# Kernel optimization log

Measured on AMD Instinct MI355X. Metric: run time of the kernel, lower is better.

The kernel has to match this reference:

```python
import jax, jax.numpy as jnp
import numpy as np

GB_TAU = 1.0
_NOISE_KEY = jax.random.key(42)


def setup_inputs() -> dict:
    key = jax.random.key(0)
    kq, kk, kv = jax.random.split(key, 3)
    n_genes, n_latent, d_k, n_cells = 16384, 4096, 64, 1024
    query = jax.random.normal(kq, (n_genes, d_k), dtype=jnp.float32)
    key_t = jax.random.normal(kk, (n_latent, d_k), dtype=jnp.float32)
    value = jax.random.normal(kv, (n_latent, n_cells), dtype=jnp.float32)
    return {"query": query, "key": key_t, "value": value}


def _gumbel_noise(shape, dtype):
    # standard Gumbel(0,1): -log(-log(U)), U ~ Uniform(0,1)
    u = jax.random.uniform(_NOISE_KEY, shape, dtype=dtype,
                           minval=jnp.finfo(dtype).tiny, maxval=1.0)
    return -jnp.log(-jnp.log(u))


def reference(query, key, value):
    d_k = query.shape[-1]
    # [n_genes, n_latent] scaled dot-product scores
    scores = jnp.matmul(query, key.T) / jnp.sqrt(jnp.asarray(d_k, query.dtype))
    # gumbel_softmax(hard=False): softmax((logits + g) / tau, axis=-1)
    g = _gumbel_noise(scores.shape, scores.dtype)
    p_attn = jax.nn.softmax((scores + g) / GB_TAU, axis=-1)
    out = jnp.matmul(p_attn, value)  # [n_genes, n_cells]
    return out, p_attn
```

## Files before the change

kernel.cpp:

```cpp
#include <hip/hip_runtime.h>
#include <cstdint>
#include <cstddef>

#define N_GENES  16384
#define N_LATENT 4096
#define D_K      64
#define N_CELLS  1024

#define NOISE_PARTITIONABLE 1

typedef __attribute__((ext_vector_type(8))) short bf16x8;
typedef __attribute__((ext_vector_type(4))) float f32x4;

__device__ __forceinline__ uint32_t rotl32(uint32_t x, int r) {
  return (x << r) | (x >> (32 - r));
}

__device__ __forceinline__ void threefry2x32(uint32_t c0, uint32_t c1,
                                             uint32_t& o0, uint32_t& o1) {
  const uint32_t ks0 = 0u, ks1 = 42u, ks2 = 0u ^ 42u ^ 0x1BD11BDAu;
  uint32_t x0 = c0 + ks0;
  uint32_t x1 = c1 + ks1;
#define TFR(r) { x0 += x1; x1 = rotl32(x1, r); x1 ^= x0; }
  TFR(13) TFR(15) TFR(26) TFR(6)
  x0 += ks1; x1 += ks2 + 1u;
  TFR(17) TFR(29) TFR(16) TFR(24)
  x0 += ks2; x1 += ks0 + 2u;
  TFR(13) TFR(15) TFR(26) TFR(6)
  x0 += ks0; x1 += ks1 + 3u;
  TFR(17) TFR(29) TFR(16) TFR(24)
  x0 += ks1; x1 += ks2 + 4u;
  TFR(13) TFR(15) TFR(26) TFR(6)
  x0 += ks2; x1 += ks0 + 5u;
#undef TFR
  o0 = x0; o1 = x1;
}

__device__ __forceinline__ uint32_t rand_bits(uint32_t m) {
#if NOISE_PARTITIONABLE
  uint32_t b0, b1;
  threefry2x32(0u, m, b0, b1);
  return b0 ^ b1;
#else
  const uint32_t h = 1u << 25;
  uint32_t b0, b1;
  if (m < h) { threefry2x32(m, m + h, b0, b1); return b0; }
  else       { threefry2x32(m - h, m, b0, b1); return b1; }
#endif
}

__device__ __forceinline__ float fastlog(float x) {
  float r;
  asm("v_log_f32 %0, %1" : "=v"(r) : "v"(x));
  return r * 0.69314718055994531f;
}

__device__ __forceinline__ float gumbel_noise(uint32_t m) {
  uint32_t bits = rand_bits(m);
  float f = __uint_as_float((bits >> 9) | 0x3f800000u) - 1.0f;
  float u = f + 1.17549435e-38f;
  float t = -fastlog(u);
  return -fastlog(t);
}

__device__ __forceinline__ ushort f2bf(float x) {
  uint32_t u = __float_as_uint(x);
  uint32_t r = (u + 0x7FFFu + ((u >> 16) & 1u)) >> 16;
  return (ushort)r;
}

__device__ __forceinline__ float bf2f(uint32_t us) {
  return __uint_as_float(us << 16);
}

__device__ __forceinline__ void split1(float x, ushort& h, ushort& l) {
  ushort hb = f2bf(x);
  float hf = __uint_as_float((uint32_t)hb << 16);
  h = hb;
  l = f2bf(x - hf);
}

__device__ __forceinline__ int swz(int row, int kcol) {
  return row * 64 + (((kcol >> 3) ^ (row & 7)) << 3) + (kcol & 7);
}

__global__ __launch_bounds__(256) void k_logexp(const float* __restrict__ Q,
                                                const float* __restrict__ Kk,
                                                ushort* __restrict__ Pe,
                                                float* __restrict__ Sp) {
  __shared__ ushort Qh[64 * 64], Ql[64 * 64], Kh[64 * 64], Kl[64 * 64];
  const int t = threadIdx.x;
  const int bm = blockIdx.x, bn = blockIdx.y;
  const float4* Q4 = (const float4*)(Q + ((size_t)bm << 12));
  const float4* K4 = (const float4*)(Kk + ((size_t)bn << 12));
#pragma unroll
  for (int i = 0; i < 4; ++i) {
    int idx = t + (i << 8);
    int r = idx >> 4;
    int k0 = (idx & 15) << 2;
    int sidx = swz(r, k0);
    float4 a = Q4[idx];
    ushort4 h, lo;
    split1(a.x * 0.125f, h.x, lo.x); split1(a.y * 0.125f, h.y, lo.y);
    split1(a.z * 0.125f, h.z, lo.z); split1(a.w * 0.125f, h.w, lo.w);
    *(ushort4*)&Qh[sidx] = h; *(ushort4*)&Ql[sidx] = lo;
    float4 b = K4[idx];
    split1(b.x, h.x, lo.x); split1(b.y, h.y, lo.y);
    split1(b.z, h.z, lo.z); split1(b.w, h.w, lo.w);
    *(ushort4*)&Kh[sidx] = h; *(ushort4*)&Kl[sidx] = lo;
  }
  __syncthreads();

  const int l = t & 63, w = t >> 6;
  const int wm = (w >> 1) << 5, wn = (w & 1) << 5;
  const int fr = l & 15;
  const int seg = l >> 4;
  const int koff = seg << 3;
  f32x4 acc[2][2] = {};
#pragma unroll
  for (int kseg = 0; kseg < 2; ++kseg) {
    bf16x8 ah[2], al[2], bh[2], bl[2];
    const int kc = kseg * 32 + koff;
#pragma unroll
    for (int m = 0; m < 2; ++m) {
      int row = wm + m * 16 + fr;
      int sidx = swz(row, kc);
      ah[m] = *(const bf16x8*)&Qh[sidx];
      al[m] = *(const bf16x8*)&Ql[sidx];
    }
#pragma unroll
    for (int n = 0; n < 2; ++n) {
      int row = wn + n * 16 + fr;
      int sidx = swz(row, kc);
      bh[n] = *(const bf16x8*)&Kh[sidx];
      bl[n] = *(const bf16x8*)&Kl[sidx];
    }
#pragma unroll
    for (int m = 0; m < 2; ++m)
#pragma unroll
      for (int n = 0; n < 2; ++n) {
        acc[m][n] = __builtin_amdgcn_mfma_f32_16x16x32_bf16(
            ah[m], bh[n], acc[m][n], 0, 0, 0);
        acc[m][n] = __builtin_amdgcn_mfma_f32_16x16x32_bf16(
            ah[m], bl[n], acc[m][n], 0, 0, 0);
        acc[m][n] = __builtin_amdgcn_mfma_f32_16x16x32_bf16(
            al[m], bh[n], acc[m][n], 0, 0, 0);
      }
  }

  const int gr0 = (bm << 6) + wm + (seg << 2);
  const int gc0 = (bn << 6) + wn + fr;
  float sloc[2][4] = {};
#pragma unroll
  for (int m = 0; m < 2; ++m)
#pragma unroll
    for (int n = 0; n < 2; ++n) {
      int col = gc0 + n * 16;
#pragma unroll
      for (int j = 0; j < 4; ++j) {
        int row = gr0 + m * 16 + j;
        uint32_t mb = (uint32_t)row * 4096u + (uint32_t)col;
        float e;
        asm("v_exp_f32 %0, %1" : "=v"(e)
            : "v"((acc[m][n][j] + gumbel_noise(mb)) * 1.4426950408889634f));
        Pe[(size_t)row * 4096 + col] = f2bf(e);
        sloc[m][j] += e;
      }
    }
  __shared__ float part[64][2];
#pragma unroll
  for (int m = 0; m < 2; ++m)
#pragma unroll
    for (int j = 0; j < 4; ++j) {
      float s = sloc[m][j];
      s += __shfl_xor(s, 1, 64); s += __shfl_xor(s, 2, 64);
      s += __shfl_xor(s, 4, 64); s += __shfl_xor(s, 8, 64);
      if (fr == 0) part[wm + m * 16 + (seg << 2) + j][wn >> 5] = s;
    }
  __syncthreads();
  if (t < 64)
    Sp[((size_t)(bm << 6) + t) * 64 + bn] = part[t][0] + part[t][1];
}

__global__ __launch_bounds__(256) void k_rowinv(const float* __restrict__ Sp,
                                                float* __restrict__ inv) {
  int r = blockIdx.x * 256 + threadIdx.x;
  const float4* s4 = (const float4*)(Sp + (size_t)r * 64);
  float s = 0.f;
#pragma unroll
  for (int i = 0; i < 16; ++i) {
    float4 v = s4[i];
    s += (v.x + v.y) + (v.z + v.w);
  }
  inv[r] = 1.0f / s;
}

__global__ __launch_bounds__(256) void k_pwrite(const ushort* __restrict__ Pe,
                                                const float* __restrict__ inv,
                                                float* __restrict__ P) {
  size_t i8 = (size_t)blockIdx.x * 256 + threadIdx.x;
  int row = (int)(i8 >> 9);
  float iv = inv[row];
  uint4 u = *(const uint4*)(Pe + i8 * 8);
  float4 o0, o1;
  o0.x = bf2f(u.x & 0xFFFFu) * iv; o0.y = bf2f(u.x >> 16) * iv;
  o0.z = bf2f(u.y & 0xFFFFu) * iv; o0.w = bf2f(u.y >> 16) * iv;
  o1.x = bf2f(u.z & 0xFFFFu) * iv; o1.y = bf2f(u.z >> 16) * iv;
  o1.z = bf2f(u.w & 0xFFFFu) * iv; o1.w = bf2f(u.w >> 16) * iv;
  *(float4*)(P + i8 * 8) = o0;
  *(float4*)(P + i8 * 8 + 4) = o1;
}

__global__ __launch_bounds__(256) void k_vt(const float* __restrict__ V,
                                            ushort* __restrict__ VT) {
  __shared__ ushort tile[64][68];
  const int t = threadIdx.x;
  const int k0 = blockIdx.x << 6, n0 = blockIdx.y << 6;
#pragma unroll
  for (int i = 0; i < 16; ++i) {
    int idx = t + (i << 8);
    int kr = idx >> 6;
    int c = idx & 63;
    tile[c][kr] = f2bf(V[(size_t)(k0 + kr) * 1024 + n0 + c]);
  }
  __syncthreads();
#pragma unroll
  for (int i = 0; i < 8; ++i) {
    int idx = t + (i << 8);
    int n = idx >> 5, kp = idx & 31;
    ushort2 o;
    o.x = tile[n][2 * kp];
    o.y = tile[n][2 * kp + 1];
    ((ushort2*)&VT[(size_t)(n0 + n) * 4096 + k0])[kp] = o;
  }
}

__device__ __forceinline__ void llds16(void* lds, const void* g) {
  __builtin_amdgcn_global_load_lds(
      (const __attribute__((address_space(1))) uint32_t*)g,
      (__attribute__((address_space(3))) uint32_t*)lds, 16, 0, 0);
}

__device__ __forceinline__ void stage_kt(ushort* ldsA, ushort* ldsB,
                                         const ushort* gA, const ushort* gB,
                                         int t) {
#pragma unroll
  for (int i = 0; i < 4; ++i) {
    int cid = (i << 9) + t;
    int row = cid >> 3, g = cid & 7;
    int gs = g ^ (row & 7);
    llds16(ldsA + (size_t)cid * 8, gA + (size_t)row * 4096 + gs * 8);
  }
#pragma unroll
  for (int i = 0; i < 4; ++i) {
    int cid = (i << 9) + t;
    int row = cid >> 3, g = cid & 7;
    int gs = g ^ (row & 7);
    llds16(ldsB + (size_t)cid * 8, gB + (size_t)row * 4096 + gs * 8);
  }
}

__global__ __launch_bounds__(512, 2) void k_pv3(const ushort* __restrict__ Pe,
                                                const ushort* __restrict__ VT,
                                                const float* __restrict__ inv,
                                                float* __restrict__ O) {
  __shared__ ushort lds[2][2][256 * 64];
  const int t = threadIdx.x;
  const int b = blockIdx.x;
  const int xcd = b & 7, idx = b >> 3;
  const int by = xcd * 8 + (idx >> 2);
  const int bx = idx & 3;
  const int base_m = by << 8, base_n = bx << 8;
  const int l = t & 63, w = t >> 6;
  const int wm = w >> 2, wn = w & 3;
  const int fr = l & 15, seg = l >> 4;

  const ushort* gA = Pe + (size_t)base_m * 4096;
  const ushort* gB = VT + (size_t)base_n * 4096;

  f32x4 acc[8][4] = {};

  stage_kt(lds[0][0], lds[0][1], gA, gB, t);

#define LDA_H(mh)                                                            \
  {                                                                          \
    _Pragma("unroll") for (int m = 0; m < 4; ++m)                            \
        _Pragma("unroll") for (int kk = 0; kk < 2; ++kk) {                   \
      int row = wm * 128 + (mh)*64 + m * 16 + fr;                            \
      a[m][kk] = *(const bf16x8*)&A[row * 64 +                               \
                                    ((((kk << 2) + seg) ^ (row & 7)) << 3)]; \
    }                                                                        \
  }
#define LDB_H(dst, nh)                                                       \
  {                                                                          \
    _Pragma("unroll") for (int n = 0; n < 2; ++n)                            \
        _Pragma("unroll") for (int kk = 0; kk < 2; ++kk) {                   \
      int row = wn * 64 + (nh)*32 + n * 16 + fr;                             \
      dst[n][kk] = *(const bf16x8*)&B[row * 64 +                             \
                                    ((((kk << 2) + seg) ^ (row & 7)) << 3)]; \
    }                                                                        \
  }
#define QUAD(mh, nh, bb)                                                     \
  {                                                                          \
    __builtin_amdgcn_s_setprio(1);                                           \
    _Pragma("unroll") for (int m = 0; m < 4; ++m)                            \
        _Pragma("unroll") for (int n = 0; n < 2; ++n)                        \
            _Pragma("unroll") for (int kk = 0; kk < 2; ++kk)                 \
        acc[(mh)*4 + m][(nh)*2 + n] = __builtin_amdgcn_mfma_f32_16x16x32_bf16( \
            a[m][kk], bb[n][kk], acc[(mh)*4 + m][(nh)*2 + n], 0, 0, 0);      \
    __builtin_amdgcn_s_setprio(0);                                           \
    __builtin_amdgcn_s_barrier();                                            \
  }

  for (int it = 0; it < 64; ++it) {
    const int slot = it & 1;
    const int ktn = (it < 63) ? it + 1 : it;
    stage_kt(lds[slot ^ 1][0], lds[slot ^ 1][1],
             gA + ktn * 64, gB + ktn * 64, t);
    asm volatile("s_waitcnt vmcnt(8)" ::: "memory");
    __builtin_amdgcn_s_barrier();
    const ushort* A = lds[slot][0];
    const ushort* B = lds[slot][1];
    bf16x8 a[4][2], b0[2][2], b1[2][2];
    LDA_H(0) LDB_H(b0, 0)
    QUAD(0, 0, b0)
    LDB_H(b1, 1)
    QUAD(0, 1, b1)
    LDA_H(1)
    QUAD(1, 0, b0)
    QUAD(1, 1, b1)
  }

#pragma unroll
  for (int mi = 0; mi < 8; ++mi) {
    int row_ = base_m + wm * 128 + mi * 16 + seg * 4;
#pragma unroll
    for (int j = 0; j < 4; ++j) {
      float iv = inv[row_ + j];
#pragma unroll
      for (int ni = 0; ni < 4; ++ni)
        O[(size_t)(row_ + j) * 1024 + base_n + wn * 64 + ni * 16 + fr] =
            acc[mi][ni][j] * iv;
    }
  }
#undef LDA_H
#undef LDB_H
#undef QUAD
}

__global__ __launch_bounds__(256) void k_logits_raw(const float* __restrict__ Q,
                                                    const float* __restrict__ Kk,
                                                    float* __restrict__ L) {
  __shared__ float Qt[64][68];
  __shared__ float Kt[64][68];
  const int t = threadIdx.x;
  const int bm = blockIdx.x, bn = blockIdx.y;
  const float4* Q4 = (const float4*)(Q + ((size_t)bm << 12));
  const float4* K4 = (const float4*)(Kk + ((size_t)bn << 12));
#pragma unroll
  for (int i = 0; i < 4; ++i) {
    int idx = t + (i << 8);
    int r = idx >> 4;
    int k0 = (idx & 15) << 2;
    float4 a = Q4[idx];
    Qt[k0 + 0][r] = a.x; Qt[k0 + 1][r] = a.y;
    Qt[k0 + 2][r] = a.z; Qt[k0 + 3][r] = a.w;
    float4 b = K4[idx];
    Kt[k0 + 0][r] = b.x; Kt[k0 + 1][r] = b.y;
    Kt[k0 + 2][r] = b.z; Kt[k0 + 3][r] = b.w;
  }
  __syncthreads();
  const int r0 = (t >> 4) << 2;
  const int c0 = (t & 15) << 2;
  float acc[4][4] = {};
#pragma unroll 8
  for (int k = 0; k < 64; ++k) {
    float a[4], b[4];
    *(float4*)a = *(const float4*)&Qt[k][r0];
    *(float4*)b = *(const float4*)&Kt[k][c0];
#pragma unroll
    for (int i = 0; i < 4; ++i)
#pragma unroll
      for (int j = 0; j < 4; ++j)
        acc[i][j] = fmaf(a[i], b[j], acc[i][j]);
  }
  const int gr = (bm << 6) + r0;
  const int gc = (bn << 6) + c0;
#pragma unroll
  for (int i = 0; i < 4; ++i) {
    uint32_t mb = (uint32_t)(gr + i) * 4096u + (uint32_t)gc;
    float4 o;
    o.x = acc[i][0] * 0.125f + gumbel_noise(mb + 0u);
    o.y = acc[i][1] * 0.125f + gumbel_noise(mb + 1u);
    o.z = acc[i][2] * 0.125f + gumbel_noise(mb + 2u);
    o.w = acc[i][3] * 0.125f + gumbel_noise(mb + 3u);
    *(float4*)&L[(size_t)(gr + i) * 4096 + gc] = o;
  }
}

__global__ __launch_bounds__(256) void k_softmax(float* __restrict__ P) {
  const int row = blockIdx.x;
  float* Lr = P + ((size_t)row << 12);
  const int t = threadIdx.x;
  float4 v[4];
#pragma unroll
  for (int i = 0; i < 4; ++i) v[i] = ((const float4*)Lr)[t + (i << 8)];
  float mx = -3.402823466e38f;
#pragma unroll
  for (int i = 0; i < 4; ++i)
    mx = fmaxf(mx, fmaxf(fmaxf(v[i].x, v[i].y), fmaxf(v[i].z, v[i].w)));
#pragma unroll
  for (int o = 1; o < 64; o <<= 1) mx = fmaxf(mx, __shfl_xor(mx, o, 64));
  __shared__ float redm[4];
  __shared__ float reds[4];
  const int lane = t & 63, w = t >> 6;
  if (lane == 0) redm[w] = mx;
  __syncthreads();
  mx = fmaxf(fmaxf(redm[0], redm[1]), fmaxf(redm[2], redm[3]));
  float s = 0.f;
#pragma unroll
  for (int i = 0; i < 4; ++i) {
    v[i].x = expf(v[i].x - mx); v[i].y = expf(v[i].y - mx);
    v[i].z = expf(v[i].z - mx); v[i].w = expf(v[i].w - mx);
    s += (v[i].x + v[i].y) + (v[i].z + v[i].w);
  }
#pragma unroll
  for (int o = 1; o < 64; o <<= 1) s += __shfl_xor(s, o, 64);
  if (lane == 0) reds[w] = s;
  __syncthreads();
  const float inv = 1.0f / (((reds[0] + reds[1]) + (reds[2] + reds[3])));
#pragma unroll
  for (int i = 0; i < 4; ++i) {
    v[i].x *= inv; v[i].y *= inv; v[i].z *= inv; v[i].w *= inv;
    ((float4*)Lr)[t + (i << 8)] = v[i];
  }
}

__global__ __launch_bounds__(256) void k_pv(const float* __restrict__ P,
                                            const float* __restrict__ V,
                                            float* __restrict__ O) {
  __shared__ float Pt[32][132];
  __shared__ float Vs[32][132];
  const int t = threadIdx.x;
  const int base_m = blockIdx.x << 7;
  const int base_n = blockIdx.y << 7;
  const int tr = (t >> 4) << 2;
  const int tc = (t & 15) << 2;
  float acc[2][2][4][4] = {};
  for (int k0 = 0; k0 < N_LATENT; k0 += 32) {
#pragma unroll
    for (int i = 0; i < 4; ++i) {
      int idx = t + (i << 8);
      int m = idx >> 3;
      int kk = (idx & 7) << 2;
      float4 a = *(const float4*)&P[(size_t)(base_m + m) * 4096 + (k0 + kk)];
      Pt[kk + 0][m] = a.x; Pt[kk + 1][m] = a.y;
      Pt[kk + 2][m] = a.z; Pt[kk + 3][m] = a.w;
      int kv = idx >> 5;
      int n4 = (idx & 31) << 2;
      *(float4*)&Vs[kv][n4] =
          *(const float4*)&V[(size_t)(k0 + kv) * 1024 + base_n + n4];
    }
    __syncthreads();
#pragma unroll 4
    for (int k = 0; k < 32; ++k) {
      float a[2][4], b[2][4];
      *(float4*)a[0] = *(const float4*)&Pt[k][tr];
      *(float4*)a[1] = *(const float4*)&Pt[k][tr + 64];
      *(float4*)b[0] = *(const float4*)&Vs[k][tc];
      *(float4*)b[1] = *(const float4*)&Vs[k][tc + 64];
#pragma unroll
      for (int ih = 0; ih < 2; ++ih)
#pragma unroll
        for (int jh = 0; jh < 2; ++jh)
#pragma unroll
          for (int i = 0; i < 4; ++i)
#pragma unroll
            for (int j = 0; j < 4; ++j)
              acc[ih][jh][i][j] =
                  fmaf(a[ih][i], b[jh][j], acc[ih][jh][i][j]);
    }
    __syncthreads();
  }
#pragma unroll
  for (int ih = 0; ih < 2; ++ih)
#pragma unroll
    for (int i = 0; i < 4; ++i) {
      int row = base_m + (ih << 6) + tr + i;
#pragma unroll
      for (int jh = 0; jh < 2; ++jh) {
        float4 o;
        o.x = acc[ih][jh][i][0]; o.y = acc[ih][jh][i][1];
        o.z = acc[ih][jh][i][2]; o.w = acc[ih][jh][i][3];
        *(float4*)&O[(size_t)row * 1024 + base_n + (jh << 6) + tc] = o;
      }
    }
}

extern "C" void kernel_launch(void* const* d_in, const int* in_sizes, int n_in,
                              void* d_out, int out_size, void* d_ws, size_t ws_size,
                              hipStream_t stream) {
  const float* Q = (const float*)d_in[0];
  const float* K = (const float*)d_in[1];
  const float* V = (const float*)d_in[2];
  float* O = (float*)d_out;
  float* P = O + (size_t)N_GENES * N_CELLS;

  const size_t pe_bytes = (size_t)N_GENES * N_LATENT * 2;
  const size_t vt_bytes = (size_t)N_CELLS * N_LATENT * 2;
  const size_t inv_bytes = (size_t)N_GENES * 4;
  const bool fast = ws_size >= pe_bytes + vt_bytes + inv_bytes;

  if (fast) {
    ushort* Pe = (ushort*)d_ws;
    ushort* VT = (ushort*)((char*)d_ws + pe_bytes);
    float* inv = (float*)((char*)d_ws + pe_bytes + vt_bytes);
    float* Sp = P;

    k_logexp<<<dim3(N_GENES / 64, N_LATENT / 64), 256, 0, stream>>>(Q, K, Pe, Sp);
    k_rowinv<<<N_GENES / 256, 256, 0, stream>>>(Sp, inv);
    k_vt<<<dim3(N_LATENT / 64, N_CELLS / 64), 256, 0, stream>>>(V, VT);
    k_pwrite<<<(int)((size_t)N_GENES * N_LATENT / 8 / 256), 256, 0, stream>>>(Pe, inv, P);
    k_pv3<<<256, 512, 0, stream>>>(Pe, VT, inv, O);
  } else {
    k_logits_raw<<<dim3(N_GENES / 64, N_LATENT / 64), 256, 0, stream>>>(Q, K, P);
    k_softmax<<<N_GENES, 256, 0, stream>>>(P);
    k_pv<<<dim3(N_GENES / 128, N_CELLS / 128), 256, 0, stream>>>(P, V, O);
  }
}
```

Before: 399.8 us.

## Fuse normalized P write into PV GEMM and use hardware bf16/log instructions

Removes the separate k_pwrite pass by having the PV GEMM kernel convert its already-staged bf16 P tile from LDS to fp32, scale it by the row inverse, and write it out each k-iteration. This saves a full re-read of the bf16 P buffer from global memory and one kernel launch. The logexp kernel also switches to v_cvt_pk_bf16_f32, alignbit rotates and a direct v_log/v_exp Gumbel path to cut ALU work. The cost is extra global stores and barriers inside the GEMM loop, which may disturb MFMA scheduling.

```diff
diff --git a/kernel.cpp b/kernel.cpp
--- a/kernel.cpp
+++ b/kernel.cpp
@@ -13,7 +13,7 @@
 typedef __attribute__((ext_vector_type(4))) float f32x4;
 
 __device__ __forceinline__ uint32_t rotl32(uint32_t x, int r) {
-  return (x << r) | (x >> (32 - r));
+  return __builtin_amdgcn_alignbit(x, x, 32 - r);
 }
 
 __device__ __forceinline__ void threefry2x32(uint32_t c0, uint32_t c1,
@@ -73,11 +73,10 @@
   return __uint_as_float(us << 16);
 }
 
-__device__ __forceinline__ void split1(float x, ushort& h, ushort& l) {
-  ushort hb = f2bf(x);
-  float hf = __uint_as_float((uint32_t)hb << 16);
-  h = hb;
-  l = f2bf(x - hf);
+__device__ __forceinline__ uint32_t cvtpk_bf16(float lo, float hi) {
+  uint32_t r;
+  asm("v_cvt_pk_bf16_f32 %0, %1, %2" : "=v"(r) : "v"(lo), "v"(hi));
+  return r;
 }
 
 __device__ __forceinline__ int swz(int row, int kcol) {
@@ -100,14 +99,28 @@
     int k0 = (idx & 15) << 2;
     int sidx = swz(r, k0);
     float4 a = Q4[idx];
-    ushort4 h, lo;
-    split1(a.x * 0.125f, h.x, lo.x); split1(a.y * 0.125f, h.y, lo.y);
-    split1(a.z * 0.125f, h.z, lo.z); split1(a.w * 0.125f, h.w, lo.w);
-    *(ushort4*)&Qh[sidx] = h; *(ushort4*)&Ql[sidx] = lo;
+    a.x *= 0.125f; a.y *= 0.125f; a.z *= 0.125f; a.w *= 0.125f;
+    {
+      uint32_t h01 = cvtpk_bf16(a.x, a.y), h23 = cvtpk_bf16(a.z, a.w);
+      float lx = a.x - __uint_as_float(h01 << 16);
+      float ly = a.y - __uint_as_float(h01 & 0xffff0000u);
+      float lz = a.z - __uint_as_float(h23 << 16);
+      float lw = a.w - __uint_as_float(h23 & 0xffff0000u);
+      uint32_t l01 = cvtpk_bf16(lx, ly), l23 = cvtpk_bf16(lz, lw);
+      *(uint2*)&Qh[sidx] = make_uint2(h01, h23);
+      *(uint2*)&Ql[sidx] = make_uint2(l01, l23);
+    }
     float4 b = K4[idx];
-    split1(b.x, h.x, lo.x); split1(b.y, h.y, lo.y);
-    split1(b.z, h.z, lo.z); split1(b.w, h.w, lo.w);
-    *(ushort4*)&Kh[sidx] = h; *(ushort4*)&Kl[sidx] = lo;
+    {
+      uint32_t h01 = cvtpk_bf16(b.x, b.y), h23 = cvtpk_bf16(b.z, b.w);
+      float lx = b.x - __uint_as_float(h01 << 16);
+      float ly = b.y - __uint_as_float(h01 & 0xffff0000u);
+      float lz = b.z - __uint_as_float(h23 << 16);
+      float lw = b.w - __uint_as_float(h23 & 0xffff0000u);
+      uint32_t l01 = cvtpk_bf16(lx, ly), l23 = cvtpk_bf16(lz, lw);
+      *(uint2*)&Kh[sidx] = make_uint2(h01, h23);
+      *(uint2*)&Kl[sidx] = make_uint2(l01, l23);
+    }
   }
   __syncthreads();
 
@@ -148,6 +161,8 @@
       }
   }
 
+  const float LOG2E = 1.44269504088896340f;
+  const float NLN2 = -0.69314718055994531f;
   const int gr0 = (bm << 6) + wm + (seg << 2);
   const int gc0 = (bn << 6) + wn + fr;
   float sloc[2][4] = {};
@@ -156,16 +171,31 @@
 #pragma unroll
     for (int n = 0; n < 2; ++n) {
       int col = gc0 + n * 16;
+      uint32_t mbase = (uint32_t)(gr0 + m * 16) * 4096u + (uint32_t)col;
+      float e[4];
 #pragma unroll
       for (int j = 0; j < 4; ++j) {
-        int row = gr0 + m * 16 + j;
-        uint32_t mb = (uint32_t)row * 4096u + (uint32_t)col;
-        float e;
-        asm("v_exp_f32 %0, %1" : "=v"(e)
-            : "v"((acc[m][n][j] + gumbel_noise(mb)) * 1.4426950408889634f));
-        Pe[(size_t)row * 4096 + col] = f2bf(e);
-        sloc[m][j] += e;
+        uint32_t bits = rand_bits(mbase + (uint32_t)j * 4096u);
+        float f = __uint_as_float((bits >> 9) | 0x3f800000u) - 1.0f;
+        float u = f + 1.17549435e-38f;
+        float lgu;
+        asm("v_log_f32 %0, %1" : "=v"(lgu) : "v"(u));
+        float tq = lgu * NLN2;
+        float lgt;
+        asm("v_log_f32 %0, %1" : "=v"(lgt) : "v"(tq));
+        float ee;
+        asm("v_exp_f32 %0, %1" : "=v"(ee)
+            : "v"(fmaf(acc[m][n][j], LOG2E, -lgt)));
+        e[j] = ee;
+        sloc[m][j] += ee;
       }
+      uint32_t p01 = cvtpk_bf16(e[0], e[1]);
+      uint32_t p23 = cvtpk_bf16(e[2], e[3]);
+      size_t base = (size_t)(gr0 + m * 16) * 4096 + col;
+      Pe[base] = (ushort)p01;
+      Pe[base + 4096] = (ushort)(p01 >> 16);
+      Pe[base + 2 * 4096] = (ushort)p23;
+      Pe[base + 3 * 4096] = (ushort)(p23 >> 16);
     }
   __shared__ float part[64][2];
 #pragma unroll
@@ -193,22 +223,6 @@
     s += (v.x + v.y) + (v.z + v.w);
   }
   inv[r] = 1.0f / s;
-}
-
-__global__ __launch_bounds__(256) void k_pwrite(const ushort* __restrict__ Pe,
-                                                const float* __restrict__ inv,
-                                                float* __restrict__ P) {
-  size_t i8 = (size_t)blockIdx.x * 256 + threadIdx.x;
-  int row = (int)(i8 >> 9);
-  float iv = inv[row];
-  uint4 u = *(const uint4*)(Pe + i8 * 8);
-  float4 o0, o1;
-  o0.x = bf2f(u.x & 0xFFFFu) * iv; o0.y = bf2f(u.x >> 16) * iv;
-  o0.z = bf2f(u.y & 0xFFFFu) * iv; o0.w = bf2f(u.y >> 16) * iv;
-  o1.x = bf2f(u.z & 0xFFFFu) * iv; o1.y = bf2f(u.z >> 16) * iv;
-  o1.z = bf2f(u.w & 0xFFFFu) * iv; o1.w = bf2f(u.w >> 16) * iv;
-  *(float4*)(P + i8 * 8) = o0;
-  *(float4*)(P + i8 * 8 + 4) = o1;
 }
 
 __global__ __launch_bounds__(256) void k_vt(const float* __restrict__ V,
@@ -260,9 +274,10 @@
   }
 }
 
-__global__ __launch_bounds__(512, 2) void k_pv3(const ushort* __restrict__ Pe,
+__global__ __launch_bounds__(512, 2) void k_pv4(const ushort* __restrict__ Pe,
                                                 const ushort* __restrict__ VT,
                                                 const float* __restrict__ inv,
+                                                float* __restrict__ P,
                                                 float* __restrict__ O) {
   __shared__ ushort lds[2][2][256 * 64];
   const int t = threadIdx.x;
@@ -278,6 +293,13 @@
   const ushort* gA = Pe + (size_t)base_m * 4096;
   const ushort* gB = VT + (size_t)base_n * 4096;
 
+  const int pr_loc = bx * 64 + (t >> 3);
+  const int pw_g = t & 7;
+  const int pw_off = pr_loc * 64 + ((pw_g ^ (pr_loc & 7)) << 3);
+  const int pw_row = base_m + pr_loc;
+  const float iv_pw = inv[pw_row];
+  float* Pdst = P + (size_t)pw_row * 4096 + pw_g * 8;
+
   f32x4 acc[8][4] = {};
 
   stage_kt(lds[0][0], lds[0][1], gA, gB, t);
@@ -300,7 +322,7 @@
                                     ((((kk << 2) + seg) ^ (row & 7)) << 3)]; \
     }                                                                        \
   }
-#define QUAD(mh, nh, bb)                                                     \
+#define QUADM(mh, nh, bb)                                                    \
   {                                                                          \
     __builtin_amdgcn_s_setprio(1);                                           \
     _Pragma("unroll") for (int m = 0; m < 4; ++m)                            \
@@ -309,7 +331,6 @@
         acc[(mh)*4 + m][(nh)*2 + n] = __builtin_amdgcn_mfma_f32_16x16x32_bf16( \
             a[m][kk], bb[n][kk], acc[(mh)*4 + m][(nh)*2 + n], 0, 0, 0);      \
     __builtin_amdgcn_s_setprio(0);                                           \
-    __builtin_amdgcn_s_barrier();                                            \
   }
 
   for (int it = 0; it < 64; ++it) {
@@ -323,12 +344,28 @@
     const ushort* B = lds[slot][1];
     bf16x8 a[4][2], b0[2][2], b1[2][2];
     LDA_H(0) LDB_H(b0, 0)
-    QUAD(0, 0, b0)
+    QUADM(0, 0, b0)
+    __builtin_amdgcn_s_barrier();
     LDB_H(b1, 1)
-    QUAD(0, 1, b1)
+    QUADM(0, 1, b1)
+    __builtin_amdgcn_s_barrier();
     LDA_H(1)
-    QUAD(1, 0, b0)
-    QUAD(1, 1, b1)
+    QUADM(1, 0, b0)
+    __builtin_amdgcn_s_barrier();
+    QUADM(1, 1, b1)
+    {
+      bf16x8 pv_ = *(const bf16x8*)&A[pw_off];
+      const uint32_t* pu = (const uint32_t*)&pv_;
+      float4 o0, o1;
+      uint32_t w0 = pu[0], w1 = pu[1], w2 = pu[2], w3 = pu[3];
+      o0.x = bf2f(w0) * iv_pw;        o0.y = bf2f(w0 >> 16) * iv_pw;
+      o0.z = bf2f(w1) * iv_pw;        o0.w = bf2f(w1 >> 16) * iv_pw;
+      o1.x = bf2f(w2) * iv_pw;        o1.y = bf2f(w2 >> 16) * iv_pw;
+      o1.z = bf2f(w3) * iv_pw;        o1.w = bf2f(w3 >> 16) * iv_pw;
+      *(float4*)(Pdst + (size_t)it * 64) = o0;
+      *(float4*)(Pdst + (size_t)it * 64 + 4) = o1;
+    }
+    __builtin_amdgcn_s_barrier();
   }
 
 #pragma unroll
@@ -345,7 +382,7 @@
   }
 #undef LDA_H
 #undef LDB_H
-#undef QUAD
+#undef QUADM
 }
 
 __global__ __launch_bounds__(256) void k_logits_raw(const float* __restrict__ Q,
@@ -520,8 +557,7 @@
     k_logexp<<<dim3(N_GENES / 64, N_LATENT / 64), 256, 0, stream>>>(Q, K, Pe, Sp);
     k_rowinv<<<N_GENES / 256, 256, 0, stream>>>(Sp, inv);
     k_vt<<<dim3(N_LATENT / 64, N_CELLS / 64), 256, 0, stream>>>(V, VT);
-    k_pwrite<<<(int)((size_t)N_GENES * N_LATENT / 8 / 256), 256, 0, stream>>>(Pe, inv, P);
-    k_pv3<<<256, 512, 0, stream>>>(Pe, VT, inv, O);
+    k_pv4<<<256, 512, 0, stream>>>(Pe, VT, inv, P, O);
   } else {
     k_logits_raw<<<dim3(N_GENES / 64, N_LATENT / 64), 256, 0, stream>>>(Q, K, P);
     k_softmax<<<N_GENES, 256, 0, stream>>>(P);
```

Measured after the change: 357.7 us. -10.5%, faster.
